# Performance work log

Measured on AMD Instinct MI355X. Metric: run time of the kernel, lower is better.

Reference implementation:

```python
import jax, jax.numpy as jnp
from jax import lax
import numpy as np

H, W, C = 128, 128, 1024          # backbone feature map (stride-16, ResNet C4)
STRIDE = 16
NUM_ANCHORS = 9                   # 3 scales x 3 ratios
IOU_THRESHOLD = 0.7
SCORE_THRESHOLD = 0.5


def _make_anchors():
    scales = np.array([128.0, 256.0, 512.0], np.float32)
    ratios = np.array([0.5, 1.0, 2.0], np.float32)
    hs = (scales[:, None] * np.sqrt(ratios)[None, :]).reshape(-1)   # [9]
    ws = (scales[:, None] / np.sqrt(ratios)[None, :]).reshape(-1)   # [9]
    cy = (np.arange(H, dtype=np.float32) + 0.5) * STRIDE
    cx = (np.arange(W, dtype=np.float32) + 0.5) * STRIDE
    anc = np.zeros((H, W, NUM_ANCHORS, 4), np.float32)
    anc[..., 0] = cy[:, None, None]
    anc[..., 1] = cx[None, :, None]
    anc[..., 2] = hs
    anc[..., 3] = ws
    return anc.reshape(-1, 4)      # [N,4] as (cy, cx, h, w)


def _conv(x, w, b):
    return lax.conv_general_dilated(
        x, w, (1, 1), 'SAME', dimension_numbers=('NHWC', 'HWIO', 'NHWC')) + b


def _rpn_head(features, w1, b1, w2, b2, w_score, b_score, w_box, b_box):
    x = jax.nn.relu(features)
    x = _conv(x, w1, b1)
    x = jax.nn.relu(x)
    x = _conv(x, w2, b2)
    scores = jax.nn.sigmoid(_conv(x, w_score, b_score))   # [1,H,W,9]
    shifts = _conv(x, w_box, b_box)                        # [1,H,W,36]
    return scores.reshape(-1, 1), shifts.reshape(-1, 4)


def _decode(shifts, anchors):
    acy, acx, ah, aw = anchors[:, 0], anchors[:, 1], anchors[:, 2], anchors[:, 3]
    dy, dx, dh, dw = shifts[:, 0], shifts[:, 1], shifts[:, 2], shifts[:, 3]
    cy = acy + dy * ah
    cx = acx + dx * aw
    h = ah * jnp.exp(dh)
    w = aw * jnp.exp(dw)
    y1 = jnp.clip(cy - 0.5 * h, 0.0, H * STRIDE)
    x1 = jnp.clip(cx - 0.5 * w, 0.0, W * STRIDE)
    y2 = jnp.clip(cy + 0.5 * h, 0.0, H * STRIDE)
    x2 = jnp.clip(cx + 0.5 * w, 0.0, W * STRIDE)
    return jnp.stack([y1, x1, y2, x2], axis=-1)            # [N,4]


def _nms(boxes, scores, max_out):
    """Greedy NMS like tf.image.non_max_suppression, fixed-size padded output."""
    n = boxes.shape[0]
    areas = (boxes[:, 2] - boxes[:, 0]) * (boxes[:, 3] - boxes[:, 1])

    def body(state):
        suppressed, sel, count = state
        masked = jnp.where(suppressed, -jnp.inf, scores)
        i = jnp.argmax(masked)
        valid = masked[i] >= SCORE_THRESHOLD
        sel = sel.at[count].set(jnp.where(valid, i.astype(jnp.int32), -1))
        count = count + valid.astype(jnp.int32)
        b = boxes[i]
        iy = jnp.maximum(0.0, jnp.minimum(b[2], boxes[:, 2]) - jnp.maximum(b[0], boxes[:, 0]))
        ix = jnp.maximum(0.0, jnp.minimum(b[3], boxes[:, 3]) - jnp.maximum(b[1], boxes[:, 1]))
        inter = iy * ix
        iou = inter / (areas[i] + areas - inter + 1e-9)
        new_sup = (suppressed | (iou > IOU_THRESHOLD)).at[i].set(True)
        suppressed = jnp.where(valid, new_sup, jnp.ones_like(suppressed))
        return suppressed, sel, count

    def cond(state):
        suppressed, sel, count = state
        return (count < max_out) & (~jnp.all(suppressed))

    sel0 = jnp.full((max_out,), -1, jnp.int32)
    sup0 = jnp.zeros((n,), bool)
    _, sel, _ = lax.while_loop(cond, body, (sup0, sel0, jnp.int32(0)))
    valid = sel >= 0
    idx = jnp.where(valid, sel, 0)
    return boxes[idx] * valid[:, None], scores[idx] * valid, valid


def setup_inputs() -> dict:
    key = jax.random.key(0)
    ks = jax.random.split(key, 5)
    def init_w(k, shape, fan_in, scale=1.0):
        return jax.random.normal(k, shape, jnp.float32) * (scale / np.sqrt(fan_in))
    features = jax.random.normal(ks[0], (1, H, W, C), jnp.float32)
    w1 = init_w(ks[1], (3, 3, C, 512), 9 * C)
    b1 = jnp.zeros((512,), jnp.float32)
    w2 = init_w(ks[2], (3, 3, 512, 512), 9 * 512)
    b2 = jnp.zeros((512,), jnp.float32)
    w_score = init_w(ks[3], (1, 1, 512, NUM_ANCHORS), 512)
    b_score = jnp.zeros((NUM_ANCHORS,), jnp.float32)
    w_box = init_w(ks[4], (1, 1, 512, 4 * NUM_ANCHORS), 512, scale=0.1)
    b_box = jnp.zeros((4 * NUM_ANCHORS,), jnp.float32)
    return {"features": features, "w1": w1, "b1": b1, "w2": w2, "b2": b2,
            "w_score": w_score, "b_score": b_score,
            "w_box": w_box, "b_box": b_box, "region_limit": 300}


def reference(features, w1, b1, w2, b2, w_score, b_score, w_box, b_box, region_limit):
    pred_scores, pred_shifts = _rpn_head(features, w1, b1, w2, b2,
                                         w_score, b_score, w_box, b_box)
    anchors = jnp.asarray(_make_anchors())
    boxes = _decode(pred_shifts, anchors)
    return _nms(boxes, pred_scores[:, 0], int(region_limit))
```

## Files before the change

kernel.cpp:

```cpp
#include <hip/hip_runtime.h>

#define HW 128
#define COUTC 512
#define NB 4097
#define NSEL 300
#define T_TOP 4096
#define TW 64
#define FAST_N 1024

typedef _Float16 half8 __attribute__((ext_vector_type(8)));
typedef _Float16 half4v __attribute__((ext_vector_type(4)));
typedef float floatx4 __attribute__((ext_vector_type(4)));

#define NWS_A1H   ((size_t)0)
#define NWS_A1L   ((size_t)34611200)
#define NWS_W1H   ((size_t)69222400)
#define NWS_W1L   ((size_t)78659584)
#define NWS_A2H   ((size_t)88096768)
#define NWS_A2L   ((size_t)105402368)
#define NWS_W2H   ((size_t)122707968)
#define NWS_W2L   ((size_t)127426560)
#define NWS_X2    ((size_t)132145152)
#define NWS_BOXES ((size_t)165699584)
#define NWS_KEYS  ((size_t)168058880)
#define NWS_SKEYS ((size_t)169238528)
#define NWS_HIST  ((size_t)170418176)
#define NWS_CUR   ((size_t)170434816)
#define NWS_CNT   ((size_t)170451456)
#define NWS_BASE  ((size_t)170451712)
#define NWS_TOTAL ((size_t)170468352)

#define WS_X1     ((size_t)0)
#define WS_X2     ((size_t)33554432)
#define WS_BOXES  ((size_t)67108864)
#define WS_KEYS   ((size_t)69468160)
#define WS_SKEYS  ((size_t)70647808)
#define WS_HIST   ((size_t)71827456)
#define WS_CUR    ((size_t)71844096)
#define WS_CNT    ((size_t)71860736)
#define WS_BASE   ((size_t)71860992)

__device__ __forceinline__ void glds16(const void* g, void* l) {
    __builtin_amdgcn_global_load_lds(
        (const __attribute__((address_space(1))) void*)g,
        (__attribute__((address_space(3))) void*)l, 16, 0, 0);
}


__global__ __launch_bounds__(256) void convert_feat_kernel(
    const float* __restrict__ feat, _Float16* __restrict__ ah, _Float16* __restrict__ al)
{
    __shared__ __align__(16) _Float16 lh[130 * 32];
    __shared__ __align__(16) _Float16 ll[130 * 32];
    int pr = blockIdx.x;
    int chunk = blockIdx.y;
    int t = threadIdx.x;
    int c  = t & 31;
    int pg = t >> 5;
    bool interior = (pr >= 1 && pr <= 128);
    if (interior) {
        for (int px = pg; px < 128; px += 8) {
            float x = feat[((size_t)(pr - 1) * 128 + px) * 1024 + chunk * 32 + c];
            x = fmaxf(x, 0.f);
            _Float16 hi = (_Float16)x;
            lh[(px + 1) * 32 + c] = hi;
            ll[(px + 1) * 32 + c] = (_Float16)(x - (float)hi);
        }
    } else {
        for (int px = pg; px < 128; px += 8) {
            lh[(px + 1) * 32 + c] = (_Float16)0.f;
            ll[(px + 1) * 32 + c] = (_Float16)0.f;
        }
    }
    if (t < 32) {
        lh[t] = (_Float16)0.f;          ll[t] = (_Float16)0.f;
        lh[129 * 32 + t] = (_Float16)0.f; ll[129 * 32 + t] = (_Float16)0.f;
    }
    __syncthreads();
    size_t base = (size_t)pr * 133120 + (size_t)chunk * 4160;
    for (int i = t; i < 520; i += 256) {
        int sub = i / 130;
        int pc  = i - sub * 130;
        *(float4*)&ah[base + sub * 1040 + pc * 8] = *(const float4*)&lh[pc * 32 + sub * 8];
        *(float4*)&al[base + sub * 1040 + pc * 8] = *(const float4*)&ll[pc * 32 + sub * 8];
    }
}

template<int CIN>
__device__ __forceinline__ void convert_w_body(
    int b, const float* __restrict__ w, _Float16* __restrict__ wh, _Float16* __restrict__ wl)
{
    constexpr int NU = CIN / 8;
    int gid = b * 256 + threadIdx.x;
    int oc = gid & 511;
    int rest = gid >> 9;
    int u = rest & (NU - 1);
    int tap = rest / NU;
    if (tap >= 9) return;
    int k0 = u * 8;
    half8 vh, vl;
    #pragma unroll
    for (int j = 0; j < 8; ++j) {
        float v = w[((size_t)tap * CIN + k0 + j) * 512 + oc] * 64.f;
        _Float16 hi = (_Float16)v;
        vh[j] = hi;
        vl[j] = (_Float16)(v - (float)hi);
    }
    size_t o = (size_t)tap * CIN * 512 + (size_t)(k0 >> 5) * 16384
             + (size_t)((k0 >> 3) & 3) * 4096 + (size_t)oc * 8;
    *(half8*)(wh + o) = vh;
    *(half8*)(wl + o) = vl;
}

__global__ __launch_bounds__(256) void prep_kernel(
    const float* __restrict__ w1, _Float16* __restrict__ w1h, _Float16* __restrict__ w1l,
    const float* __restrict__ w2, _Float16* __restrict__ w2h, _Float16* __restrict__ w2l,
    const float* __restrict__ w_s, const float* __restrict__ w_b,
    _Float16* __restrict__ wbh, _Float16* __restrict__ wbl,
    _Float16* __restrict__ a2h, _Float16* __restrict__ a2l)
{
    int b = blockIdx.x;
    if (b < 2304) { convert_w_body<1024>(b, w1, w1h, w1l); return; }
    if (b < 3456) { convert_w_body<512>(b - 2304, w2, w2h, w2l); return; }
    if (b < 3584) {
        int gid = (b - 3456) * 256 + threadIdx.x;
        int n = gid & 63;
        int k = gid >> 6;
        float v = 0.f;
        if (n < 9)       v = w_s[k * 9 + n] * 64.f;
        else if (n < 45) v = w_b[k * 36 + (n - 9)] * 64.f;
        _Float16 hi = (_Float16)v;
        size_t o = (size_t)(k >> 5) * 2048 + (size_t)((k >> 3) & 3) * 512 + (size_t)n * 8 + (k & 7);
        wbh[o] = hi;
        wbl[o] = (_Float16)(v - (float)hi);
        return;
    }
    {
        int i = b - 3584;
        int pr, pc;
        if (i < 130)      { pr = 0;        pc = i; }
        else if (i < 260) { pr = 129;      pc = i - 130; }
        else if (i < 388) { pr = i - 259;  pc = 0; }
        else              { pr = i - 387;  pc = 129; }
        int t = threadIdx.x;
        if (t >= 128) return;
        _Float16* dst = (t & 64) ? a2l : a2h;
        int u = t & 63;
        size_t o = (size_t)pr * 66560 + (size_t)(u >> 2) * 4160 + (size_t)(u & 3) * 1040 + (size_t)pc * 8;
        *(float4*)(dst + o) = make_float4(0.f, 0.f, 0.f, 0.f);
    }
}

template<int CIN, bool PAD>
__global__ __launch_bounds__(256) void conv_mfma_kernel(
    const _Float16* __restrict__ ah, const _Float16* __restrict__ al,
    const _Float16* __restrict__ wh, const _Float16* __restrict__ wl,
    const float* __restrict__ bias,
    _Float16* __restrict__ oh, _Float16* __restrict__ ol)
{
    constexpr int ROWSTR = CIN * 130;
    constexpr int TAPW   = CIN * 512;
    __shared__ __align__(16) _Float16 lds[32768];

    int bx = blockIdx.x;
    int h  = bx & 127;
    int n0 = (bx >> 7) << 7;

    int tid  = threadIdx.x;
    int wave = tid >> 6;
    int lane = tid & 63;
    int fr = lane & 15;
    int fq = lane >> 4;

    int aoff0 = fq * 1040 + (32 * wave + fr) * 8;
    int aoff1 = aoff0 + 128;
    int boff0 = fq * 4096 + (n0 + 32 * wave + fr) * 8;
    int boff1 = boff0 + 128;

    int wm = wave & 1, wn = wave >> 1;

    floatx4 acc[4][4];
    #pragma unroll
    for (int i = 0; i < 4; ++i)
        #pragma unroll
        for (int j = 0; j < 4; ++j)
            acc[i][j] = (floatx4){0.f, 0.f, 0.f, 0.f};

    #pragma unroll
    for (int tap = 0; tap < 9; ++tap) {
        int dy = tap / 3 - 1, dx = tap % 3 - 1;
        const _Float16* gAh = ah + (size_t)(h + dy + 1) * ROWSTR + (dx + 1) * 8;
        const _Float16* gAl = al + (size_t)(h + dy + 1) * ROWSTR + (dx + 1) * 8;
        const _Float16* gBh = wh + (size_t)tap * TAPW;
        const _Float16* gBl = wl + (size_t)tap * TAPW;

        for (int kc = 0; kc < CIN; kc += 64) {
            #pragma unroll
            for (int s = 0; s < 2; ++s) {
                int ab = ((kc >> 5) + s) * 4160;
                int bb = ((kc >> 5) + s) * 16384;
                _Float16* A0 = lds +          s * 4096 + 2 * wave * 512;
                _Float16* L0 = lds + 8192  +  s * 4096 + 2 * wave * 512;
                _Float16* B0 = lds + 16384 +  s * 4096 + 2 * wave * 512;
                _Float16* C0 = lds + 24576 +  s * 4096 + 2 * wave * 512;
                glds16(gAh + ab + aoff0, A0);
                glds16(gAh + ab + aoff1, A0 + 512);
                glds16(gAl + ab + aoff0, L0);
                glds16(gAl + ab + aoff1, L0 + 512);
                glds16(gBh + bb + boff0, B0);
                glds16(gBh + bb + boff1, B0 + 512);
                glds16(gBl + bb + boff0, C0);
                glds16(gBl + bb + boff1, C0 + 512);
            }
            __syncthreads();

            #pragma unroll
            for (int s = 0; s < 2; ++s) {
                const _Float16* rAh = lds +          s * 4096 + wm * 2048 + fq * 128 + fr * 8;
                const _Float16* rAl = rAh + 8192;
                const _Float16* rBh = lds + 16384 +  s * 4096 + wn * 2048 + fq * 128 + fr * 8;
                const _Float16* rBl = rBh + 8192;

                half8 fah[4], fal[4], fbh[4], fbl[4];
                #pragma unroll
                for (int i = 0; i < 4; ++i) {
                    fah[i] = *(const half8*)(rAh + i * 512);
                    fal[i] = *(const half8*)(rAl + i * 512);
                    fbh[i] = *(const half8*)(rBh + i * 512);
                    fbl[i] = *(const half8*)(rBl + i * 512);
                }
                #pragma unroll
                for (int i = 0; i < 4; ++i)
                    #pragma unroll
                    for (int j = 0; j < 4; ++j)
                        acc[i][j] = __builtin_amdgcn_mfma_f32_16x16x32_f16(fah[i], fbh[j], acc[i][j], 0, 0, 0);
                #pragma unroll
                for (int i = 0; i < 4; ++i)
                    #pragma unroll
                    for (int j = 0; j < 4; ++j)
                        acc[i][j] = __builtin_amdgcn_mfma_f32_16x16x32_f16(fah[i], fbl[j], acc[i][j], 0, 0, 0);
                #pragma unroll
                for (int i = 0; i < 4; ++i)
                    #pragma unroll
                    for (int j = 0; j < 4; ++j)
                        acc[i][j] = __builtin_amdgcn_mfma_f32_16x16x32_f16(fal[i], fbh[j], acc[i][j], 0, 0, 0);
            }
            __syncthreads();
        }
    }

    const float scale = 1.f / 64.f;
    int em = 64 * wm + fq * 4;
    int en = 64 * wn + fr;
    #pragma unroll
    for (int j = 0; j < 4; ++j) {
        int oc = n0 + en + 16 * j;
        float b = bias[oc];
        #pragma unroll
        for (int i = 0; i < 4; ++i) {
            #pragma unroll
            for (int r = 0; r < 4; ++r) {
                int w = em + 16 * i + r;
                float v = fmaf(acc[i][j][r], scale, b);
                if (PAD) {
                    v = fmaxf(v, 0.f);
                    _Float16 hi = (_Float16)v;
                    size_t o = (size_t)(h + 1) * 66560 + (size_t)(oc >> 5) * 4160
                             + (size_t)((oc >> 3) & 3) * 1040 + (size_t)(w + 1) * 8 + (oc & 7);
                    oh[o] = hi;
                    ol[o] = (_Float16)(v - (float)hi);
                } else {
                    _Float16 hi = (_Float16)v;
                    size_t o = (size_t)h * 65536 + (size_t)(oc >> 5) * 4096
                             + (size_t)((oc >> 3) & 3) * 1024 + (size_t)w * 8 + (oc & 7);
                    oh[o] = hi;
                    ol[o] = (_Float16)(v - (float)hi);
                }
            }
        }
    }
}

__device__ __forceinline__ void decode_emit(
    int gi, float z, float dyv, float dxv, float dhv, float dwv,
    float4* __restrict__ boxes, unsigned long long* __restrict__ keys,
    int* __restrict__ cnt, int* __restrict__ hist)
{
    int a = gi % 9;
    int pix = gi / 9;
    int h = pix >> 7, w = pix & 127;
    float sc  = (a < 3) ? 128.f : ((a < 6) ? 256.f : 512.f);
    int r = a - (a / 3) * 3;
    float ratio = (r == 0) ? 0.5f : ((r == 1) ? 1.f : 2.f);
    float sr = sqrtf(ratio);
    float ahh = sc * sr, aww = sc / sr;
    float acy = ((float)h + 0.5f) * 16.f;
    float acx = ((float)w + 0.5f) * 16.f;
    float cy = fmaf(dyv, ahh, acy);
    float cx = fmaf(dxv, aww, acx);
    float hh = ahh * expf(dhv);
    float ww = aww * expf(dwv);
    float y1 = fminf(fmaxf(cy - 0.5f * hh, 0.f), 2048.f);
    float x1 = fminf(fmaxf(cx - 0.5f * ww, 0.f), 2048.f);
    float y2 = fminf(fmaxf(cy + 0.5f * hh, 0.f), 2048.f);
    float x2 = fminf(fmaxf(cx + 0.5f * ww, 0.f), 2048.f);
    boxes[gi] = make_float4(y1, x1, y2, x2);
    float s = 1.f / (1.f + expf(-z));
    if (s >= 0.5f) {
        unsigned u = __float_as_uint(s);
        unsigned d = 0x3F800000u - u;
        unsigned long long key = ((unsigned long long)d << 18) | (unsigned)gi;
        int p = atomicAdd(cnt, 1);
        keys[p] = key;
        atomicAdd(&hist[d >> 11], 1);
    }
}

__global__ __launch_bounds__(256) void heads_mfma_kernel(
    const _Float16* __restrict__ xh, const _Float16* __restrict__ xl,
    const _Float16* __restrict__ wbh, const _Float16* __restrict__ wbl,
    const float* __restrict__ b_s, const float* __restrict__ b_b,
    float4* __restrict__ boxes, unsigned long long* __restrict__ keys,
    int* __restrict__ cnt, int* __restrict__ hist)
{
    __shared__ __align__(16) char smem[24576];
    _Float16* sAh = (_Float16*)smem;
    _Float16* sAl = (_Float16*)(smem + 8192);
    _Float16* sBh = (_Float16*)(smem + 16384);
    _Float16* sBl = (_Float16*)(smem + 20480);
    float* outs = (float*)smem;
    __shared__ float sb[48];

    int tid  = threadIdx.x;
    int wave = tid >> 6;
    int lane = tid & 63;
    int fr = lane & 15;
    int fq = lane >> 4;
    if (tid < 48) sb[tid] = (tid < 9) ? b_s[tid] : ((tid < 45) ? b_b[tid - 9] : 0.f);

    int h = blockIdx.x;
    int wm = wave & 1, wn = wave >> 1;

    floatx4 acc[4][2];
    #pragma unroll
    for (int i = 0; i < 4; ++i)
        #pragma unroll
        for (int j = 0; j < 2; ++j)
            acc[i][j] = (floatx4){0.f, 0.f, 0.f, 0.f};

    for (int kc = 0; kc < 16; ++kc) {
        const _Float16* gxh = xh + (size_t)h * 65536 + kc * 4096;
        const _Float16* gxl = xl + (size_t)h * 65536 + kc * 4096;
        glds16(gxh + tid * 8,        sAh + tid * 8);
        glds16(gxh + 2048 + tid * 8, sAh + 2048 + tid * 8);
        glds16(gxl + tid * 8,        sAl + tid * 8);
        glds16(gxl + 2048 + tid * 8, sAl + 2048 + tid * 8);
        glds16(wbh + kc * 2048 + tid * 8, sBh + tid * 8);
        glds16(wbl + kc * 2048 + tid * 8, sBl + tid * 8);
        __syncthreads();

        half8 fah[4], fal[4], fbh[2], fbl[2];
        #pragma unroll
        for (int i = 0; i < 4; ++i) {
            int px = wm * 64 + 16 * i + fr;
            int aaddr = fq * 1024 + px * 8;
            fah[i] = *(const half8*)(sAh + aaddr);
            fal[i] = *(const half8*)(sAl + aaddr);
        }
        #pragma unroll
        for (int j = 0; j < 2; ++j) {
            int n = wn * 32 + 16 * j + fr;
            int baddr = fq * 512 + n * 8;
            fbh[j] = *(const half8*)(sBh + baddr);
            fbl[j] = *(const half8*)(sBl + baddr);
        }
        #pragma unroll
        for (int i = 0; i < 4; ++i)
            #pragma unroll
            for (int j = 0; j < 2; ++j) {
                acc[i][j] = __builtin_amdgcn_mfma_f32_16x16x32_f16(fah[i], fbh[j], acc[i][j], 0, 0, 0);
                acc[i][j] = __builtin_amdgcn_mfma_f32_16x16x32_f16(fah[i], fbl[j], acc[i][j], 0, 0, 0);
                acc[i][j] = __builtin_amdgcn_mfma_f32_16x16x32_f16(fal[i], fbh[j], acc[i][j], 0, 0, 0);
            }
        __syncthreads();
    }

    const float scale = 1.f / 64.f;
    #pragma unroll
    for (int i = 0; i < 4; ++i)
        #pragma unroll
        for (int j = 0; j < 2; ++j)
            #pragma unroll
            for (int r = 0; r < 4; ++r) {
                int px = wm * 64 + 16 * i + fq * 4 + r;
                int n = wn * 32 + 16 * j + fr;
                if (n < 48)
                    outs[px * 48 + n] = fmaf(acc[i][j][r], scale, sb[n]);
            }
    __syncthreads();

    if (tid < 128) {
        int p = tid;
        #pragma unroll
        for (int a = 0; a < 9; ++a) {
            float z   = outs[p * 48 + a];
            float dyv = outs[p * 48 + 9 + 4 * a + 0];
            float dxv = outs[p * 48 + 9 + 4 * a + 1];
            float dhv = outs[p * 48 + 9 + 4 * a + 2];
            float dwv = outs[p * 48 + 9 + 4 * a + 3];
            int gi = (h * 128 + p) * 9 + a;
            decode_emit(gi, z, dyv, dxv, dhv, dwv, boxes, keys, cnt, hist);
        }
    }
}

template<int CIN, bool RELU_IN, bool RELU_OUT>
__global__ __launch_bounds__(256) void conv3x3_kernel(
    const float* __restrict__ in, const float* __restrict__ wgt,
    const float* __restrict__ bias, float* __restrict__ out)
{
    __shared__ float As[32][68];
    __shared__ float Bs[32][64];
    int bx = blockIdx.x;
    int mtile = bx & 255, ntile = bx >> 8;
    int h = mtile >> 1, w0 = (mtile & 1) << 6, n0 = ntile << 6;
    int tid = threadIdx.x, ty = tid >> 4, tx = tid & 15;
    float acc[4][4] = {{0.f}};
    const int KTOT = 9 * CIN;
    for (int k0 = 0; k0 < KTOT; k0 += 32) {
        int tap = k0 / CIN, icb = k0 % CIN;
        int dy = tap / 3 - 1, dx = tap % 3 - 1;
        int row = h + dy;
        bool rowok = ((unsigned)row < HW);
        {
            int pix = tid >> 3, cs = (tid & 7) << 2;
            #pragma unroll
            for (int p = 0; p < 2; ++p) {
                int px = pix + p * 32;
                int wcol = w0 + px + dx;
                float4 v = make_float4(0.f, 0.f, 0.f, 0.f);
                if (rowok && (unsigned)wcol < HW) {
                    v = *(const float4*)&in[((size_t)row * HW + wcol) * CIN + icb + cs];
                    if (RELU_IN) {
                        v.x = fmaxf(v.x, 0.f); v.y = fmaxf(v.y, 0.f);
                        v.z = fmaxf(v.z, 0.f); v.w = fmaxf(v.w, 0.f);
                    }
                }
                As[cs + 0][px] = v.x; As[cs + 1][px] = v.y;
                As[cs + 2][px] = v.z; As[cs + 3][px] = v.w;
            }
        }
        {
            int kr = tid >> 4, nc = (tid & 15) << 2;
            #pragma unroll
            for (int p = 0; p < 2; ++p) {
                int k = kr + p * 16;
                *(float4*)&Bs[k][nc] = *(const float4*)&wgt[(size_t)(k0 + k) * COUTC + n0 + nc];
            }
        }
        __syncthreads();
        #pragma unroll
        for (int kk = 0; kk < 32; ++kk) {
            float4 a = *(const float4*)&As[kk][ty << 2];
            float4 b = *(const float4*)&Bs[kk][tx << 2];
            float av[4] = {a.x, a.y, a.z, a.w};
            float bv[4] = {b.x, b.y, b.z, b.w};
            #pragma unroll
            for (int i = 0; i < 4; ++i)
                #pragma unroll
                for (int j = 0; j < 4; ++j)
                    acc[i][j] = fmaf(av[i], bv[j], acc[i][j]);
        }
        __syncthreads();
    }
    float4 bi = *(const float4*)&bias[n0 + (tx << 2)];
    float bv2[4] = {bi.x, bi.y, bi.z, bi.w};
    #pragma unroll
    for (int i = 0; i < 4; ++i) {
        float4 o;
        o.x = acc[i][0] + bv2[0]; o.y = acc[i][1] + bv2[1];
        o.z = acc[i][2] + bv2[2]; o.w = acc[i][3] + bv2[3];
        if (RELU_OUT) {
            o.x = fmaxf(o.x, 0.f); o.y = fmaxf(o.y, 0.f);
            o.z = fmaxf(o.z, 0.f); o.w = fmaxf(o.w, 0.f);
        }
        *(float4*)&out[((size_t)(h * HW) + w0 + (ty << 2) + i) * COUTC + n0 + (tx << 2)] = o;
    }
}

__global__ __launch_bounds__(256) void heads_decode_kernel(
    const float* __restrict__ x, const float* __restrict__ w_s, const float* __restrict__ b_s,
    const float* __restrict__ w_b, const float* __restrict__ b_b,
    float4* __restrict__ boxes, unsigned long long* __restrict__ keys,
    int* __restrict__ cnt, int* __restrict__ hist)
{
    __shared__ float xs[4][512];
    __shared__ float outs[4][45];
    int wave = threadIdx.x >> 6;
    int lane = threadIdx.x & 63;
    int pix  = blockIdx.x * 4 + wave;

    const float4* xp = (const float4*)&x[(size_t)pix * COUTC];
    *(float4*)&xs[wave][lane * 4]       = xp[lane];
    *(float4*)&xs[wave][256 + lane * 4] = xp[64 + lane];
    __syncthreads();

    if (lane < 45) {
        const float* wp; int stride; float acc;
        if (lane < 9) { wp = w_s + lane;       stride = 9;  acc = b_s[lane]; }
        else          { wp = w_b + (lane - 9); stride = 36; acc = b_b[lane - 9]; }
        const float* xrow = xs[wave];
        for (int k = 0; k < 512; k += 4) {
            acc = fmaf(xrow[k + 0], wp[(k + 0) * stride], acc);
            acc = fmaf(xrow[k + 1], wp[(k + 1) * stride], acc);
            acc = fmaf(xrow[k + 2], wp[(k + 2) * stride], acc);
            acc = fmaf(xrow[k + 3], wp[(k + 3) * stride], acc);
        }
        outs[wave][lane] = acc;
    }
    __syncthreads();

    if (lane < 9) {
        int a = lane;
        decode_emit(pix * 9 + a, outs[wave][a],
                    outs[wave][9 + 4 * a + 0], outs[wave][9 + 4 * a + 1],
                    outs[wave][9 + 4 * a + 2], outs[wave][9 + 4 * a + 3],
                    boxes, keys, cnt, hist);
    }
}

__global__ __launch_bounds__(256) void scan_kernel(
    const int* __restrict__ hist, int* __restrict__ base)
{
    __shared__ int tot[256];
    int t = threadIdx.x;
    int v[16];
    int s = 0;
    #pragma unroll
    for (int i = 0; i < 16; ++i) { v[i] = hist[t * 16 + i]; s += v[i]; }
    tot[t] = s;
    __syncthreads();
    for (int d = 1; d < 256; d <<= 1) {
        int x = (t >= d) ? tot[t - d] : 0;
        __syncthreads();
        tot[t] += x;
        __syncthreads();
    }
    int excl = (t == 0) ? 0 : tot[t - 1];
    #pragma unroll
    for (int i = 0; i < 16; ++i) { base[t * 16 + i] = excl; excl += v[i]; }
    if (t == 255) { base[4096] = excl; base[4097] = excl + hist[4096]; }
}

__global__ __launch_bounds__(256) void scatter_kernel(
    const unsigned long long* __restrict__ keys, const int* __restrict__ cnt,
    const int* __restrict__ base, int* __restrict__ cur,
    unsigned long long* __restrict__ skeys)
{
    int i = blockIdx.x * 256 + threadIdx.x;
    if (i < *cnt) {
        unsigned long long k = keys[i];
        int b = (int)(k >> 29);
        int p = base[b] + atomicAdd(&cur[b], 1);
        skeys[p] = k;
    }
}

__global__ __launch_bounds__(256) void sortb_kernel(
    const unsigned long long* __restrict__ skeys, const int* __restrict__ base,
    const float4* __restrict__ boxes,
    unsigned long long* __restrict__ sk2,
    float4* __restrict__ cboxes, float* __restrict__ careas)
{
    __shared__ unsigned long long sk[2048];
    int b = blockIdx.x;
    int s0 = base[b];
    int n = base[b + 1] - s0;
    if (n <= 0) return;
    int t = threadIdx.x;
    if (n <= 2048) {
        for (int i = t; i < n; i += 256) sk[i] = skeys[s0 + i];
        __syncthreads();
        for (int i = t; i < n; i += 256) {
            unsigned long long k = sk[i];
            int r = 0;
            for (int j = 0; j < n; ++j) r += (sk[j] < k) ? 1 : 0;
            int pos = s0 + r;
            sk2[pos] = k;
            if (pos < T_TOP) {
                float4 bb = boxes[k & 0x3FFFFull];
                cboxes[pos] = bb;
                careas[pos] = (bb.z - bb.x) * (bb.w - bb.y);
            }
        }
    } else {
        const unsigned long long* src = skeys + s0;
        for (int i = t; i < n; i += 256) {
            unsigned long long k = src[i];
            int r = 0;
            for (int j = 0; j < n; ++j) r += (src[j] < k) ? 1 : 0;
            int pos = s0 + r;
            sk2[pos] = k;
            if (pos < T_TOP) {
                float4 bb = boxes[k & 0x3FFFFull];
                cboxes[pos] = bb;
                careas[pos] = (bb.z - bb.x) * (bb.w - bb.y);
            }
        }
    }
}

__global__ __launch_bounds__(256) void mask_kernel(
    const float4* __restrict__ cboxes, const float* __restrict__ careas,
    unsigned long long* __restrict__ msk)
{
    int bi = blockIdx.y, bj = blockIdx.x;
    if (bj < bi) return;
    __shared__ float4 jb[256];
    __shared__ float  ja[256];
    int t = threadIdx.x;
    int j0 = bj << 8;
    jb[t] = cboxes[j0 + t];
    ja[t] = careas[j0 + t];
    __syncthreads();
    int i = (bi << 8) + t;
    float4 ci = cboxes[i];
    float ca = careas[i];
    unsigned long long word = 0;
    for (int jj = 0; jj < 256; ++jj) {
        int j = j0 + jj;
        float4 b = jb[jj];
        float iy = fmaxf(0.f, fminf(ci.z, b.z) - fmaxf(ci.x, b.x));
        float ix = fmaxf(0.f, fminf(ci.w, b.w) - fmaxf(ci.y, b.y));
        float inter = iy * ix;
        float iou = inter / (ca + ja[jj] - inter + 1e-9f);
        bool bit = (j == i) || (j > i && iou > 0.7f);
        if (bit) word |= 1ull << (jj & 63);
        if ((jj & 63) == 63) {
            msk[(size_t)i * TW + (bj << 2) + (jj >> 6)] = word;
            word = 0;
        }
    }
}

__global__ __launch_bounds__(256) void walk_kernel(
    const unsigned long long* __restrict__ sk2, const int* __restrict__ cnt,
    const float4* __restrict__ cboxes, const float* __restrict__ careas,
    const unsigned long long* __restrict__ msk, const float4* __restrict__ boxes,
    float* __restrict__ out)
{
    __shared__ unsigned long long mlds[FAST_N * 16];
    __shared__ unsigned long long sup[TW];
    __shared__ float4 sbox[NSEL];
    __shared__ float  sarea[NSEL];
    __shared__ unsigned short sellist[NSEL];
    int tid = threadIdx.x;
    for (int i = tid; i < 1800; i += 256) out[i] = 0.f;
    int total = *cnt;
    int Tc = min(total, T_TOP);
    int FN = min(Tc, FAST_N);
    for (int i = tid; i < FN * 16; i += 256) {
        mlds[i] = msk[(size_t)(i >> 4) * TW + (i & 15)];
    }
    if (tid < TW) sup[tid] = 0ull;
    __syncthreads();
    if (tid >= 64) return;
    int lane = tid;
    int sel = 0;

    {
        int p = 0;
        while (sel < NSEL) {
            int w0 = p >> 6;
            unsigned long long m = 0;
            if (lane < 16 && lane >= w0) {
                m = ~sup[lane];
                if (lane == w0) m &= (~0ull << (p & 63));
            }
            unsigned long long bal = __ballot(m != 0ull);
            if (bal == 0ull) break;
            int w = __builtin_ctzll(bal);
            int bit = __shfl(m ? __builtin_ctzll(m) : 0, w);
            int c = (w << 6) + bit;
            if (c >= FN) break;
            float4 cb = cboxes[c];
            float ca = careas[c];
            if (lane == 0) {
                unsigned long long key = sk2[c];
                out[sel * 4 + 0] = cb.x; out[sel * 4 + 1] = cb.y;
                out[sel * 4 + 2] = cb.z; out[sel * 4 + 3] = cb.w;
                out[1200 + sel] = __uint_as_float(0x3F800000u - (unsigned)(key >> 18));
                out[1500 + sel] = 1.f;
                sbox[sel] = cb;
                sarea[sel] = ca;
                sellist[sel] = (unsigned short)c;
            }
            sel++;
            if (lane < 16) sup[lane] |= mlds[c * 16 + lane];
            p = c + 1;
        }
    }

    if (sel < NSEL && Tc > FN) {
        unsigned long long acc = 0ull;
        if (lane >= 16) {
            for (int s = 0; s < sel; ++s)
                acc |= msk[(size_t)sellist[s] * TW + lane];
            sup[lane] = acc;
        }

        auto scanFrom = [&](int p) -> int {
            if (p < 0 || p >= Tc) return -1;
            int w = p >> 6;
            unsigned long long f = (~sup[w]) & (~0ull << (p & 63));
            while (f == 0ull) {
                ++w;
                if (w >= TW) return -1;
                f = ~sup[w];
            }
            int c = (w << 6) + __builtin_ctzll(f);
            return (c < Tc) ? c : -1;
        };

        unsigned long long r0 = 0, r1 = 0, r2n = 0;
        int idx = scanFrom(FN);
        if (idx >= 0) r0 = msk[(size_t)idx * TW + lane];
        int idx2 = (idx >= 0) ? scanFrom(idx + 1) : -1;
        if (idx2 >= 0) r1 = msk[(size_t)idx2 * TW + lane];

        while (idx >= 0 && sel < NSEL) {
            float4 cb = cboxes[idx];
            float ca = careas[idx];
            if (lane == 0) {
                unsigned long long key = sk2[idx];
                out[sel * 4 + 0] = cb.x; out[sel * 4 + 1] = cb.y;
                out[sel * 4 + 2] = cb.z; out[sel * 4 + 3] = cb.w;
                out[1200 + sel] = __uint_as_float(0x3F800000u - (unsigned)(key >> 18));
                out[1500 + sel] = 1.f;
                sbox[sel] = cb;
                sarea[sel] = ca;
            }
            sel++;
            if (sel >= NSEL) break;

            int idx3 = (idx2 >= 0) ? scanFrom(idx2 + 1) : -1;
            if (idx3 >= 0) r2n = msk[(size_t)idx3 * TW + lane];

            sup[lane] |= r0;

            if (idx2 >= 0) {
                unsigned long long w = sup[idx2 >> 6];
                if ((w >> (idx2 & 63)) & 1ull) {
                    idx2 = scanFrom(idx2);
                    if (idx2 >= 0) r1 = msk[(size_t)idx2 * TW + lane];
                    idx3 = (idx2 >= 0) ? scanFrom(idx2 + 1) : -1;
                    if (idx3 >= 0) r2n = msk[(size_t)idx3 * TW + lane];
                }
            }
            idx = idx2; r0 = r1;
            idx2 = idx3; r1 = r2n;
        }
    }

    if (sel < NSEL && total > T_TOP) {
        for (int i = T_TOP; i < total && sel < NSEL; ++i) {
            unsigned long long key = sk2[i];
            float4 cb = boxes[key & 0x3FFFFull];
            float ca = (cb.z - cb.x) * (cb.w - cb.y);
            int supp = 0;
            for (int t = lane; t < sel; t += 64) {
                float4 s4 = sbox[t];
                float iy = fmaxf(0.f, fminf(s4.z, cb.z) - fmaxf(s4.x, cb.x));
                float ix = fmaxf(0.f, fminf(s4.w, cb.w) - fmaxf(s4.y, cb.y));
                float inter = iy * ix;
                float iou = inter / (sarea[t] + ca - inter + 1e-9f);
                if (iou > 0.7f) supp = 1;
            }
            if (__ballot(supp) == 0ull) {
                if (lane == 0) {
                    out[sel * 4 + 0] = cb.x; out[sel * 4 + 1] = cb.y;
                    out[sel * 4 + 2] = cb.z; out[sel * 4 + 3] = cb.w;
                    out[1200 + sel] = __uint_as_float(0x3F800000u - (unsigned)(key >> 18));
                    out[1500 + sel] = 1.f;
                    sbox[sel] = cb;
                    sarea[sel] = ca;
                }
                sel++;
            }
        }
    }
}

extern "C" void kernel_launch(void* const* d_in, const int* in_sizes, int n_in,
                              void* d_out, int out_size, void* d_ws, size_t ws_size,
                              hipStream_t stream) {
    const float* feat = (const float*)d_in[0];
    const float* w1   = (const float*)d_in[1];
    const float* b1   = (const float*)d_in[2];
    const float* w2   = (const float*)d_in[3];
    const float* b2   = (const float*)d_in[4];
    const float* w_s  = (const float*)d_in[5];
    const float* b_s  = (const float*)d_in[6];
    const float* w_b  = (const float*)d_in[7];
    const float* b_b  = (const float*)d_in[8];
    float* out = (float*)d_out;
    char* ws = (char*)d_ws;

    if (ws_size >= NWS_TOTAL) {
        _Float16* a1h = (_Float16*)(ws + NWS_A1H);
        _Float16* a1l = (_Float16*)(ws + NWS_A1L);
        _Float16* w1h = (_Float16*)(ws + NWS_W1H);
        _Float16* w1l = (_Float16*)(ws + NWS_W1L);
        _Float16* a2h = (_Float16*)(ws + NWS_A2H);
        _Float16* a2l = (_Float16*)(ws + NWS_A2L);
        _Float16* w2h = (_Float16*)(ws + NWS_W2H);
        _Float16* w2l = (_Float16*)(ws + NWS_W2L);
        _Float16* xh  = (_Float16*)(ws + NWS_X2);
        _Float16* xl  = (_Float16*)(ws + NWS_X2 + 16777216);
        float4* boxes = (float4*)(ws + NWS_BOXES);
        unsigned long long* keys  = (unsigned long long*)(ws + NWS_KEYS);
        unsigned long long* skeys = (unsigned long long*)(ws + NWS_SKEYS);
        int* hist = (int*)(ws + NWS_HIST);
        int* cur  = (int*)(ws + NWS_CUR);
        int* cnt  = (int*)(ws + NWS_CNT);
        int* base = (int*)(ws + NWS_BASE);
        _Float16* wbh = (_Float16*)(ws + NWS_SKEYS);
        _Float16* wbl = (_Float16*)(ws + NWS_SKEYS + 65536);
        unsigned long long* msk = (unsigned long long*)(ws + NWS_A1H);
        float4* cbox  = (float4*)(ws + NWS_A1L);
        float*  carea = (float*)(ws + NWS_A1L + 262144);
        unsigned long long* sk2 = keys;

        hipMemsetAsync(ws + NWS_HIST, 0, (NWS_CNT - NWS_HIST) + 256, stream);
        convert_feat_kernel<<<dim3(130, 32), 256, 0, stream>>>(feat, a1h, a1l);
        prep_kernel<<<4100, 256, 0, stream>>>(w1, w1h, w1l, w2, w2h, w2l,
                                              w_s, w_b, wbh, wbl, a2h, a2l);
        conv_mfma_kernel<1024, true ><<<512, 256, 0, stream>>>(a1h, a1l, w1h, w1l, b1, a2h, a2l);
        conv_mfma_kernel< 512, false><<<512, 256, 0, stream>>>(a2h, a2l, w2h, w2l, b2, xh, xl);
        heads_mfma_kernel<<<128, 256, 0, stream>>>(xh, xl, wbh, wbl, b_s, b_b, boxes, keys, cnt, hist);
        scan_kernel<<<1, 256, 0, stream>>>(hist, base);
        scatter_kernel<<<576, 256, 0, stream>>>(keys, cnt, base, cur, skeys);
        sortb_kernel<<<NB, 256, 0, stream>>>(skeys, base, boxes, sk2, cbox, carea);
        mask_kernel<<<dim3(16, 16), 256, 0, stream>>>(cbox, carea, msk);
        walk_kernel<<<1, 256, 0, stream>>>(sk2, cnt, cbox, carea, msk, boxes, out);
    } else {
        float* x1 = (float*)(ws + WS_X1);
        float* x2 = (float*)(ws + WS_X2);
        float4* boxes = (float4*)(ws + WS_BOXES);
        unsigned long long* keys  = (unsigned long long*)(ws + WS_KEYS);
        unsigned long long* skeys = (unsigned long long*)(ws + WS_SKEYS);
        int* hist = (int*)(ws + WS_HIST);
        int* cur  = (int*)(ws + WS_CUR);
        int* cnt  = (int*)(ws + WS_CNT);
        int* base = (int*)(ws + WS_BASE);
        unsigned long long* msk = (unsigned long long*)(ws + WS_X1);
        float4* cbox  = (float4*)(ws + WS_X2);
        float*  carea = (float*)(ws + WS_X2 + 262144);
        unsigned long long* sk2 = keys;

        hipMemsetAsync(ws + WS_HIST, 0, (WS_CNT - WS_HIST) + 256, stream);
        conv3x3_kernel<1024, true,  true ><<<2048, 256, 0, stream>>>(feat, w1, b1, x1);
        conv3x3_kernel< 512, false, false><<<2048, 256, 0, stream>>>(x1,   w2, b2, x2);
        heads_decode_kernel<<<4096, 256, 0, stream>>>(x2, w_s, b_s, w_b, b_b, boxes, keys, cnt, hist);
        scan_kernel<<<1, 256, 0, stream>>>(hist, base);
        scatter_kernel<<<576, 256, 0, stream>>>(keys, cnt, base, cur, skeys);
        sortb_kernel<<<NB, 256, 0, stream>>>(skeys, base, boxes, sk2, cbox, carea);
        mask_kernel<<<dim3(16, 16), 256, 0, stream>>>(cbox, carea, msk);
        walk_kernel<<<1, 256, 0, stream>>>(sk2, cnt, cbox, carea, msk, boxes, out);
    }
}
```

Measured before the change: 900.8 us.

## Double-buffer LDS staging in conv MFMA kernel to overlap loads with compute

After: 958.3 us. 1.06x slower.

```diff
diff --git a/kernel.cpp b/kernel.cpp
--- a/kernel.cpp
+++ b/kernel.cpp
@@ -160,6 +160,8 @@
 {
     constexpr int ROWSTR = CIN * 130;
     constexpr int TAPW   = CIN * 512;
+    constexpr int KSTEPS = CIN / 32;
+    constexpr int NSTEPS = 9 * KSTEPS;
     __shared__ __align__(16) _Float16 lds[32768];
 
     int bx = blockIdx.x;
@@ -186,67 +188,69 @@
         for (int j = 0; j < 4; ++j)
             acc[i][j] = (floatx4){0.f, 0.f, 0.f, 0.f};
 
-    #pragma unroll
-    for (int tap = 0; tap < 9; ++tap) {
+    _Float16* st0 = lds + wave * 1024;
+    _Float16* st1 = lds + 16384 + wave * 1024;
+
+    auto stage = [&](int q, _Float16* S) {
+        int tap = q / KSTEPS;
+        int c32 = q - tap * KSTEPS;
         int dy = tap / 3 - 1, dx = tap % 3 - 1;
-        const _Float16* gAh = ah + (size_t)(h + dy + 1) * ROWSTR + (dx + 1) * 8;
-        const _Float16* gAl = al + (size_t)(h + dy + 1) * ROWSTR + (dx + 1) * 8;
-        const _Float16* gBh = wh + (size_t)tap * TAPW;
-        const _Float16* gBl = wl + (size_t)tap * TAPW;
-
-        for (int kc = 0; kc < CIN; kc += 64) {
+        size_t abase = (size_t)(h + dy + 1) * ROWSTR + (size_t)(dx + 1) * 8 + (size_t)c32 * 4160;
+        size_t bbase = (size_t)tap * TAPW + (size_t)c32 * 16384;
+        const _Float16* gA = ah + abase;
+        const _Float16* gL = al + abase;
+        const _Float16* gB = wh + bbase;
+        const _Float16* gC = wl + bbase;
+        glds16(gA + aoff0, S);
+        glds16(gA + aoff1, S + 512);
+        glds16(gL + aoff0, S + 4096);
+        glds16(gL + aoff1, S + 4608);
+        glds16(gB + boff0, S + 8192);
+        glds16(gB + boff1, S + 8704);
+        glds16(gC + boff0, S + 12288);
+        glds16(gC + boff1, S + 12800);
+    };
+
+    const _Float16* rd0A = lds + wm * 2048 + fq * 128 + fr * 8;
+    const _Float16* rd0B = lds + 8192 + wn * 2048 + fq * 128 + fr * 8;
+    const _Float16* rd1A = rd0A + 16384;
+    const _Float16* rd1B = rd0B + 16384;
+
+    auto compute = [&](const _Float16* rA, const _Float16* rB) {
+        half8 fah[4], fal[4], fbh[4], fbl[4];
+        #pragma unroll
+        for (int i = 0; i < 4; ++i) {
+            fah[i] = *(const half8*)(rA + i * 512);
+            fal[i] = *(const half8*)(rA + 4096 + i * 512);
+            fbh[i] = *(const half8*)(rB + i * 512);
+            fbl[i] = *(const half8*)(rB + 4096 + i * 512);
+        }
+        #pragma unroll
+        for (int i = 0; i < 4; ++i)
             #pragma unroll
-            for (int s = 0; s < 2; ++s) {
-                int ab = ((kc >> 5) + s) * 4160;
-                int bb = ((kc >> 5) + s) * 16384;
-                _Float16* A0 = lds +          s * 4096 + 2 * wave * 512;
-                _Float16* L0 = lds + 8192  +  s * 4096 + 2 * wave * 512;
-                _Float16* B0 = lds + 16384 +  s * 4096 + 2 * wave * 512;
-                _Float16* C0 = lds + 24576 +  s * 4096 + 2 * wave * 512;
-                glds16(gAh + ab + aoff0, A0);
-                glds16(gAh + ab + aoff1, A0 + 512);
-                glds16(gAl + ab + aoff0, L0);
-                glds16(gAl + ab + aoff1, L0 + 512);
-                glds16(gBh + bb + boff0, B0);
-                glds16(gBh + bb + boff1, B0 + 512);
-                glds16(gBl + bb + boff0, C0);
-                glds16(gBl + bb + boff1, C0 + 512);
-            }
-            __syncthreads();
-
+            for (int j = 0; j < 4; ++j)
+                acc[i][j] = __builtin_amdgcn_mfma_f32_16x16x32_f16(fah[i], fbh[j], acc[i][j], 0, 0, 0);
+        #pragma unroll
+        for (int i = 0; i < 4; ++i)
             #pragma unroll
-            for (int s = 0; s < 2; ++s) {
-                const _Float16* rAh = lds +          s * 4096 + wm * 2048 + fq * 128 + fr * 8;
-                const _Float16* rAl = rAh + 8192;
-                const _Float16* rBh = lds + 16384 +  s * 4096 + wn * 2048 + fq * 128 + fr * 8;
-                const _Float16* rBl = rBh + 8192;
-
-                half8 fah[4], fal[4], fbh[4], fbl[4];
-                #pragma unroll
-                for (int i = 0; i < 4; ++i) {
-                    fah[i] = *(const half8*)(rAh + i * 512);
-                    fal[i] = *(const half8*)(rAl + i * 512);
-                    fbh[i] = *(const half8*)(rBh + i * 512);
-                    fbl[i] = *(const half8*)(rBl + i * 512);
-                }
-                #pragma unroll
-                for (int i = 0; i < 4; ++i)
-                    #pragma unroll
-                    for (int j = 0; j < 4; ++j)
-                        acc[i][j] = __builtin_amdgcn_mfma_f32_16x16x32_f16(fah[i], fbh[j], acc[i][j], 0, 0, 0);
-                #pragma unroll
-                for (int i = 0; i < 4; ++i)
-                    #pragma unroll
-                    for (int j = 0; j < 4; ++j)
-                        acc[i][j] = __builtin_amdgcn_mfma_f32_16x16x32_f16(fah[i], fbl[j], acc[i][j], 0, 0, 0);
-                #pragma unroll
-                for (int i = 0; i < 4; ++i)
-                    #pragma unroll
-                    for (int j = 0; j < 4; ++j)
-                        acc[i][j] = __builtin_amdgcn_mfma_f32_16x16x32_f16(fal[i], fbh[j], acc[i][j], 0, 0, 0);
-            }
-            __syncthreads();
-        }
+            for (int j = 0; j < 4; ++j)
+                acc[i][j] = __builtin_amdgcn_mfma_f32_16x16x32_f16(fah[i], fbl[j], acc[i][j], 0, 0, 0);
+        #pragma unroll
+        for (int i = 0; i < 4; ++i)
+            #pragma unroll
+            for (int j = 0; j < 4; ++j)
+                acc[i][j] = __builtin_amdgcn_mfma_f32_16x16x32_f16(fal[i], fbh[j], acc[i][j], 0, 0, 0);
+    };
+
+    stage(0, st0);
+    __syncthreads();
+    for (int q = 0; q < NSTEPS; q += 2) {
+        stage(q + 1, st1);
+        compute(rd0A, rd0B);
+        __syncthreads();
+        if (q + 2 < NSTEPS) stage(q + 2, st0);
+        compute(rd1A, rd1B);
+        __syncthreads();
     }
 
     const float scale = 1.f / 64.f;
```
